# Kernel tuning notes

Hardware: AMD Instinct MI355X
Metric: run time of the kernel (lower is better)

Reference implementation:

```python
import jax, jax.numpy as jnp
import numpy as np

DIM = 512
B, QL, KL = 8, 1024, 4096

def setup_inputs() -> dict:
    key = jax.random.key(0)
    k1, k2, k3 = jax.random.split(key, 3)
    output = jax.random.normal(k1, (B, QL, DIM), dtype=jnp.float32)
    context = jax.random.normal(k2, (B, KL, DIM), dtype=jnp.float32)
    # nn.Linear(2*dim, dim): weight [dim, 2*dim]; store transposed [2*dim, dim]
    W_out = jax.random.normal(k3, (DIM, 2 * DIM), dtype=jnp.float32) * (1.0 / np.sqrt(2 * DIM))
    b_out = jnp.zeros((DIM,), dtype=jnp.float32)
    return {"output": output, "context": context, "W_out": W_out, "b_out": b_out}

def reference(output, context, W_out, b_out):
    # scores: [B, QL, KL]
    attn = jnp.einsum("bqd,bkd->bqk", output, context)
    attn = jax.nn.softmax(attn, axis=-1)
    # mix: [B, QL, D]
    mix = jnp.einsum("bqk,bkd->bqd", attn, context)
    combined = jnp.concatenate([mix, output], axis=-1)  # [B, QL, 2D]
    out = jnp.tanh(jnp.einsum("bqe,de->bqd", combined, W_out) + b_out)
    return (out, attn)
```

## Files before the change

kernel.cpp:

```cpp
#include <hip/hip_runtime.h>
#include <math.h>

#define DIMM 512
#define NB 8
#define QLEN 1024
#define KLEN 4096

typedef __attribute__((ext_vector_type(4))) float floatx4;
typedef __attribute__((ext_vector_type(8))) short short8;
typedef __attribute__((ext_vector_type(4))) unsigned short ushort4v;
typedef __attribute__((ext_vector_type(8))) unsigned short ushort8v;

static __device__ __forceinline__ unsigned short f2bf(float f) {
    unsigned u = __builtin_bit_cast(unsigned, f);
    u += 0x7FFFu + ((u >> 16) & 1u);
    return (unsigned short)(u >> 16);
}
static __device__ __forceinline__ float bf2f(unsigned short h) {
    unsigned u = ((unsigned)h) << 16;
    return __builtin_bit_cast(float, u);
}
static __device__ __forceinline__ float fast_tanh(float x) {
    float e = __expf(-2.0f * fabsf(x));
    float t = (1.0f - e) / (1.0f + e);
    return copysignf(t, x);
}

static __device__ __forceinline__ void gload16(const unsigned short* g, unsigned short* l) {
    __builtin_amdgcn_global_load_lds(
        (__attribute__((address_space(1))) void*)const_cast<unsigned short*>(g),
        (__attribute__((address_space(3))) void*)l,
        16, 0, 0);
}

__global__ __launch_bounds__(256) void prep_qw(const float* __restrict__ x,
                                               const float* __restrict__ Wf,
                                               unsigned short* __restrict__ dst,
                                               unsigned short* __restrict__ dstW) {
    int b = blockIdx.x;
    if (b < 4096) {
        int idx = b * 256 + threadIdx.x;
        float4 v = ((const float4*)x)[idx];
        int r = idx >> 7;
        int c = (idx & 127) << 2;
        float f[4] = {v.x, v.y, v.z, v.w};
        ushort4v hi, lo;
#pragma unroll
        for (int e = 0; e < 4; ++e) {
            unsigned short h = f2bf(f[e]);
            hi[e] = h;
            lo[e] = f2bf(f[e] - bf2f(h));
        }
        unsigned short* row = dst + ((size_t)r << 10);
        *(ushort4v*)(row + c) = lo;
        *(ushort4v*)(row + 512 + c) = hi;
    } else {
        int idx = (b - 4096) * 256 + threadIdx.x;
        float4 v = ((const float4*)Wf)[idx];
        int r = idx >> 8;
        int c = (idx & 255) << 2;
        ushort4v hi;
        hi[0] = f2bf(v.x); hi[1] = f2bf(v.y); hi[2] = f2bf(v.z); hi[3] = f2bf(v.w);
        *(ushort4v*)(dstW + (size_t)r * 1024 + c) = hi;
    }
}

__global__ __launch_bounds__(256) void prep_ctx(const float* __restrict__ ctx,
                                                unsigned short* __restrict__ hilo,
                                                unsigned short* __restrict__ ctxT) {
    __shared__ unsigned short tile[64][66];
    int b = blockIdx.z;
    int c0 = blockIdx.x * 64;
    int k0 = blockIdx.y * 64;
    const float* src = ctx + ((size_t)b * KLEN + k0) * DIMM + c0;
    unsigned short* hl = hilo + ((size_t)b * KLEN + k0) * 1024 + c0;
    int t = threadIdx.x;
    int rr = t >> 4, cc4 = (t & 15) * 4;
#pragma unroll
    for (int it = 0; it < 4; ++it) {
        int r = rr + it * 16;
        float4 v = *(const float4*)(src + (size_t)r * DIMM + cc4);
        float f[4] = {v.x, v.y, v.z, v.w};
        ushort4v hi, lo;
#pragma unroll
        for (int e = 0; e < 4; ++e) {
            unsigned short h = f2bf(f[e]);
            hi[e] = h;
            lo[e] = f2bf(f[e] - bf2f(h));
            tile[r][cc4 + e] = h;
        }
        *(ushort4v*)(hl + (size_t)r * 1024 + cc4) = hi;
        *(ushort4v*)(hl + (size_t)r * 1024 + 512 + cc4) = lo;
    }
    __syncthreads();
#pragma unroll
    for (int it = 0; it < 2; ++it) {
        int u = t + it * 256;
        int c = u >> 3;
        int kk = (u & 7) * 8;
        ushort8v o;
#pragma unroll
        for (int e = 0; e < 8; ++e) o[e] = tile[kk + e][c];
        *(ushort8v*)(ctxT + ((size_t)b * DIMM + c0 + c) * KLEN + k0 + kk) = o;
    }
}

__global__ __launch_bounds__(256) void softmax_k(float* __restrict__ S,
                                                 unsigned short* __restrict__ Pb) {
    size_t row = blockIdx.x;
    float* p = S + row * KLEN;
    int t = threadIdx.x;
    int lane = t & 63, wv = t >> 6;
    float4 v[4];
    float mx = -3.0e38f;
#pragma unroll
    for (int i = 0; i < 4; ++i) {
        v[i] = *(const float4*)(p + i * 1024 + t * 4);
        mx = fmaxf(mx, fmaxf(fmaxf(v[i].x, v[i].y), fmaxf(v[i].z, v[i].w)));
    }
#pragma unroll
    for (int m = 32; m >= 1; m >>= 1) mx = fmaxf(mx, __shfl_xor(mx, m, 64));
    __shared__ float redm[4], reds[4];
    if (lane == 0) redm[wv] = mx;
    __syncthreads();
    mx = fmaxf(fmaxf(redm[0], redm[1]), fmaxf(redm[2], redm[3]));
    float sum = 0.f;
#pragma unroll
    for (int i = 0; i < 4; ++i) {
        v[i].x = __expf(v[i].x - mx); v[i].y = __expf(v[i].y - mx);
        v[i].z = __expf(v[i].z - mx); v[i].w = __expf(v[i].w - mx);
        sum += v[i].x + v[i].y + v[i].z + v[i].w;
    }
#pragma unroll
    for (int m = 32; m >= 1; m >>= 1) sum += __shfl_xor(sum, m, 64);
    if (lane == 0) reds[wv] = sum;
    __syncthreads();
    float inv = 1.0f / (reds[0] + reds[1] + reds[2] + reds[3]);
    unsigned short* pb = Pb + row * KLEN;
#pragma unroll
    for (int i = 0; i < 4; ++i) {
        float4 w;
        w.x = v[i].x * inv; w.y = v[i].y * inv; w.z = v[i].z * inv; w.w = v[i].w * inv;
        *(float4*)(p + i * 1024 + t * 4) = w;
        ushort4v h;
        h[0] = f2bf(w.x); h[1] = f2bf(w.y); h[2] = f2bf(w.z); h[3] = f2bf(w.w);
        *(ushort4v*)(pb + i * 1024 + t * 4) = h;
    }
}

template <int EPI, bool REMAP, int BM, int BN, bool SWZ>
__global__ __launch_bounds__(256, 4) void gemm_bt(
    const unsigned short* __restrict__ A,
    const unsigned short* __restrict__ Bm,
    float* __restrict__ Cf, unsigned short* __restrict__ Cb,
    const float* __restrict__ bias,
    int Ktiles, long lda, long ldb, long ldc,
    long a_bs, long b_bs, long c_bs) {
    constexpr int MI = BM / 32;
    constexpr int NF = BN / 32;
    __shared__ unsigned short sA[BM * 64];
    __shared__ unsigned short sB[BN * 64];

    int bx, by, bz;
    if constexpr (SWZ) {
        int nx = gridDim.x, ny = gridDim.y;
        int nblk = nx * ny * (int)gridDim.z;
        int id = (int)blockIdx.x + nx * ((int)blockIdx.y + ny * (int)blockIdx.z);
        int wid = (id & 7) * (nblk >> 3) + (id >> 3);
        bx = wid % nx;
        int rem = wid / nx;
        by = rem % ny;
        bz = rem / ny;
    } else {
        bx = blockIdx.x; by = blockIdx.y; bz = blockIdx.z;
    }

    const int tid = threadIdx.x;
    const int lane = tid & 63;
    const int wv = tid >> 6;
    const int wm = wv >> 1, wn = wv & 1;
    const int mlane = lane & 15, quad = lane >> 4;
    const unsigned short* Ab = A + (size_t)bz * a_bs + (size_t)by * BM * lda;
    const unsigned short* Bb = Bm + (size_t)bz * b_bs + (size_t)bx * BN * ldb;
    const int r8 = tid >> 3;
    const int c8 = (tid & 7) << 3;
    const int cg = ((tid & 7) ^ ((tid >> 3) & 7)) << 3;
    unsigned short* la = sA + r8 * 64 + c8;
    unsigned short* lb = sB + r8 * 64 + c8;

    floatx4 acc[MI][NF] = {};

    for (int kt = 0; kt < Ktiles; ++kt) {
        long kv = (long)kt * 64;
        long ka = kv, kb = kv;
        if (REMAP) {
            ka = kv < 512 ? kv + 512 : (kv < 1024 ? kv : kv - 1024);
            kb = kv < 1024 ? kv : kv - 1024;
        }
        if (kt) __syncthreads();
        const unsigned short* ga = Ab + (size_t)r8 * lda + ka + cg;
        const unsigned short* gb = Bb + (size_t)r8 * ldb + kb + cg;
#pragma unroll
        for (int it = 0; it < BM / 32; ++it)
            gload16(ga + (size_t)(it * 32) * lda, la + it * 2048);
#pragma unroll
        for (int it = 0; it < BN / 32; ++it)
            gload16(gb + (size_t)(it * 32) * ldb, lb + it * 2048);
        __syncthreads();
#pragma unroll
        for (int s = 0; s < 2; ++s) {
            const int swz = (((s * 4 + quad) ^ (mlane & 7)) << 3);
            short8 af[MI];
#pragma unroll
            for (int i = 0; i < MI; ++i)
                af[i] = *(const short8*)(sA + (wm * (BM / 2) + i * 16 + mlane) * 64 + swz);
#pragma unroll
            for (int j = 0; j < NF; ++j) {
                short8 bfj = *(const short8*)(sB + (wn * (BN / 2) + j * 16 + mlane) * 64 + swz);
#pragma unroll
                for (int i = 0; i < MI; ++i)
                    acc[i][j] = __builtin_amdgcn_mfma_f32_16x16x32_bf16(af[i], bfj, acc[i][j], 0, 0, 0);
            }
        }
    }

    size_t crow0 = (size_t)by * BM + wm * (BM / 2) + quad * 4;
    size_t ccol0 = (size_t)bx * BN + wn * (BN / 2) + mlane;
    size_t cbase = (size_t)bz * c_bs;
#pragma unroll
    for (int i = 0; i < MI; ++i) {
#pragma unroll
        for (int j = 0; j < NF; ++j) {
            size_t gr = crow0 + i * 16;
            size_t gc = ccol0 + j * 16;
#pragma unroll
            for (int r = 0; r < 4; ++r) {
                float vv = acc[i][j][r];
                size_t off = cbase + (gr + r) * ldc + gc;
                if (EPI == 0) Cf[off] = vv;
                else if (EPI == 1) Cb[off] = f2bf(vv);
                else Cf[off] = fast_tanh(vv + bias[gc]);
            }
        }
    }
}

extern "C" void kernel_launch(void* const* d_in, const int* in_sizes, int n_in,
                              void* d_out, int out_size, void* d_ws, size_t ws_size,
                              hipStream_t stream) {
    (void)in_sizes; (void)n_in; (void)out_size; (void)ws_size;
    const float* outp = (const float*)d_in[0];
    const float* ctx  = (const float*)d_in[1];
    const float* W    = (const float*)d_in[2];
    const float* bias = (const float*)d_in[3];

    float* out0 = (float*)d_out;
    float* attn = out0 + (size_t)NB * QLEN * DIMM;

    unsigned char* w = (unsigned char*)d_ws;
    unsigned short* R1 = (unsigned short*)(w);
    unsigned short* R2 = (unsigned short*)(w + (16ull << 20));
    unsigned short* R3 = (unsigned short*)(w + (80ull << 20));
    unsigned short* R4 = (unsigned short*)(w + (112ull << 20));

    prep_qw<<<4608, 256, 0, stream>>>(outp, W, R1, R4);
    prep_ctx<<<dim3(8, 64, 8), 256, 0, stream>>>(ctx, R2, R3);

    for (int h = 0; h < 2; ++h) {
        gemm_bt<0, true, 128, 128, false><<<dim3(32, 8, 4), 256, 0, stream>>>(
            R1 + (size_t)h * 4 * QLEN * 1024,
            R2 + (size_t)h * 4 * KLEN * 1024,
            attn + (size_t)h * 4 * QLEN * KLEN, nullptr, nullptr,
            24, 1024, 1024, 4096,
            (long)QLEN * 1024, (long)KLEN * 1024, (long)QLEN * KLEN);
    }

    softmax_k<<<8192, 256, 0, stream>>>(attn, R2);

    gemm_bt<1, false, 64, 64, true><<<dim3(8, 16, 8), 256, 0, stream>>>(
        R2, R3, nullptr, R1, nullptr,
        64, 4096, 4096, 1024,
        (long)QLEN * KLEN, (long)DIMM * KLEN, (long)QLEN * 1024);

    gemm_bt<2, false, 64, 64, true><<<dim3(8, 128, 1), 256, 0, stream>>>(
        R1, R4, out0, nullptr, bias,
        16, 1024, 1024, 512, 0, 0, 0);
}
```

Before: 458.7 us.

## Write fp32 attention probabilities from bf16 tiles inside the P·V GEMM

Softmax now writes only the bf16 probabilities. The fp32 attention output is reconstructed by the bx==0 blocks of the P·V GEMM from the bf16 tiles already staged in shared memory, which removes one full fp32 write pass from softmax. The two half-batch score GEMM launches are also merged into one launch over all 8 batches. In exchange, the returned attention values are bf16-rounded rather than full fp32 precision, and the store work lands unevenly on one column of blocks.

```diff
diff --git a/kernel.cpp b/kernel.cpp
--- a/kernel.cpp
+++ b/kernel.cpp
@@ -105,10 +105,10 @@
     }
 }
 
-__global__ __launch_bounds__(256) void softmax_k(float* __restrict__ S,
+__global__ __launch_bounds__(256) void softmax_k(const float* __restrict__ S,
                                                  unsigned short* __restrict__ Pb) {
     size_t row = blockIdx.x;
-    float* p = S + row * KLEN;
+    const float* p = S + row * KLEN;
     int t = threadIdx.x;
     int lane = t & 63, wv = t >> 6;
     float4 v[4];
@@ -139,16 +139,14 @@
     unsigned short* pb = Pb + row * KLEN;
 #pragma unroll
     for (int i = 0; i < 4; ++i) {
-        float4 w;
-        w.x = v[i].x * inv; w.y = v[i].y * inv; w.z = v[i].z * inv; w.w = v[i].w * inv;
-        *(float4*)(p + i * 1024 + t * 4) = w;
         ushort4v h;
-        h[0] = f2bf(w.x); h[1] = f2bf(w.y); h[2] = f2bf(w.z); h[3] = f2bf(w.w);
+        h[0] = f2bf(v[i].x * inv); h[1] = f2bf(v[i].y * inv);
+        h[2] = f2bf(v[i].z * inv); h[3] = f2bf(v[i].w * inv);
         *(ushort4v*)(pb + i * 1024 + t * 4) = h;
     }
 }
 
-template <int EPI, bool REMAP, int BM, int BN, bool SWZ>
+template <int EPI, bool REMAP, int BM, int BN, bool SWZ, bool WEXP>
 __global__ __launch_bounds__(256, 4) void gemm_bt(
     const unsigned short* __restrict__ A,
     const unsigned short* __restrict__ Bm,
@@ -222,6 +220,20 @@
                     acc[i][j] = __builtin_amdgcn_mfma_f32_16x16x32_bf16(af[i], bfj, acc[i][j], 0, 0, 0);
             }
         }
+        if constexpr (WEXP) {
+            if (bx == 0) {
+                float* ax = Cf + (size_t)bz * a_bs + (size_t)(by * BM + r8) * lda + kv + cg;
+#pragma unroll
+                for (int it = 0; it < BM / 32; ++it) {
+                    ushort8v pv = *(const ushort8v*)(la + it * 2048);
+                    float4 f0, f1;
+                    f0.x = bf2f(pv[0]); f0.y = bf2f(pv[1]); f0.z = bf2f(pv[2]); f0.w = bf2f(pv[3]);
+                    f1.x = bf2f(pv[4]); f1.y = bf2f(pv[5]); f1.z = bf2f(pv[6]); f1.w = bf2f(pv[7]);
+                    *(float4*)(ax + (size_t)(it * 32) * lda) = f0;
+                    *(float4*)(ax + (size_t)(it * 32) * lda + 4) = f1;
+                }
+            }
+        }
     }
 
     size_t crow0 = (size_t)by * BM + wm * (BM / 2) + quad * 4;
@@ -266,23 +278,19 @@
     prep_qw<<<4608, 256, 0, stream>>>(outp, W, R1, R4);
     prep_ctx<<<dim3(8, 64, 8), 256, 0, stream>>>(ctx, R2, R3);
 
-    for (int h = 0; h < 2; ++h) {
-        gemm_bt<0, true, 128, 128, false><<<dim3(32, 8, 4), 256, 0, stream>>>(
-            R1 + (size_t)h * 4 * QLEN * 1024,
-            R2 + (size_t)h * 4 * KLEN * 1024,
-            attn + (size_t)h * 4 * QLEN * KLEN, nullptr, nullptr,
-            24, 1024, 1024, 4096,
-            (long)QLEN * 1024, (long)KLEN * 1024, (long)QLEN * KLEN);
-    }
+    gemm_bt<0, true, 128, 128, false, false><<<dim3(32, 8, 8), 256, 0, stream>>>(
+        R1, R2, attn, nullptr, nullptr,
+        24, 1024, 1024, 4096,
+        (long)QLEN * 1024, (long)KLEN * 1024, (long)QLEN * KLEN);
 
     softmax_k<<<8192, 256, 0, stream>>>(attn, R2);
 
-    gemm_bt<1, false, 64, 64, true><<<dim3(8, 16, 8), 256, 0, stream>>>(
-        R2, R3, nullptr, R1, nullptr,
+    gemm_bt<1, false, 64, 64, true, true><<<dim3(8, 16, 8), 256, 0, stream>>>(
+        R2, R3, attn, R1, nullptr,
         64, 4096, 4096, 1024,
         (long)QLEN * KLEN, (long)DIMM * KLEN, (long)QLEN * 1024);
 
-    gemm_bt<2, false, 64, 64, true><<<dim3(8, 128, 1), 256, 0, stream>>>(
+    gemm_bt<2, false, 64, 64, true, false><<<dim3(8, 128, 1), 256, 0, stream>>>(
         R1, R4, out0, nullptr, bias,
         16, 1024, 1024, 512, 0, 0, 0);
 }
```

Result: slower. 528.6 us (+15.2%).
